# Kernel tuning notes

Measured on AMD Instinct MI355X. Metric: run time of the kernel, lower is better.

The kernel has to match this reference:

```python
import jax, jax.numpy as jnp
import numpy as np

B, N, DM, H = 2, 512, 1024, 16  # batch, seq, d_model, n_heads
DEPTHS = [1, 2, 4, 8]
LAM = 0.1  # lambda_distance


def setup_inputs() -> dict:
    key = jax.random.key(0)
    ks = jax.random.split(key, 2 + 5 * len(DEPTHS))
    inp = {
        "x": jax.random.normal(ks[0], (B, N, DM), jnp.float32),
        "depth_logits": jax.random.normal(ks[1], (len(DEPTHS),), jnp.float32),
    }
    j = 2
    for i, D in enumerate(DEPTHS):
        ds = DM // D
        r = max(1, D // 4)
        inp[f"pe{i}"] = jax.random.normal(ks[j], (N, D, ds), jnp.float32) * 0.02; j += 1
        inp[f"wqkv{i}"] = jax.random.normal(ks[j], (D, ds, 3 * ds), jnp.float32) / np.sqrt(ds); j += 1
        inp[f"wo{i}"] = jax.random.normal(ks[j], (DM, DM), jnp.float32) / np.sqrt(DM); j += 1
        inp[f"fu{i}"] = jax.random.normal(ks[j], (D, r), jnp.float32) / np.sqrt(r); j += 1
        inp[f"fv{i}"] = jax.random.normal(ks[j], (r, D), jnp.float32); j += 1
    return inp


def _ring_bias(n, lam, dtype):
    # toroidal (circular) distance bias on the sequence ring, normalized by N/2
    idx = jnp.arange(n)
    diff = jnp.abs(idx[:, None] - idx[None, :])
    ring = jnp.minimum(diff, n - diff).astype(dtype)
    return -lam * ring * (2.0 / n)  # [N, N]


def _toroidal_branch(x, pe, wqkv, wo, fu, fv):
    # x: [B, N, DM]; pe: [N, D, ds]; wqkv: [D, ds, 3ds]; wo: [DM, DM]; fu@fv: [D, D]
    b, n, dm = x.shape
    d_depth, ds, _ = wqkv.shape
    hd = ds // H
    xs = x.reshape(b, n, d_depth, ds) + pe[None]          # [B, N, D, ds]
    qkv = jnp.einsum('bnds,dse->bnde', xs, wqkv)          # per-depth-slice projection
    q, k, v = jnp.split(qkv, 3, axis=-1)
    q = q.reshape(b, n, d_depth, H, hd)
    k = k.reshape(b, n, d_depth, H, hd)
    v = v.reshape(b, n, d_depth, H, hd)
    bias = _ring_bias(n, LAM, x.dtype)
    scores = jnp.einsum('bndhe,bmdhe->bdhnm', q, k) / jnp.sqrt(jnp.asarray(hd, x.dtype))
    attn = jax.nn.softmax(scores + bias, axis=-1)          # [B, D, H, N, N]
    o = jnp.einsum('bdhnm,bmdhe->bndhe', attn, v).reshape(b, n, d_depth, ds)
    mix = fu @ fv                                          # low-rank depth fusion [D, D]
    fused = jnp.einsum('df,bnfs->bnds', mix, o).reshape(b, n, dm)
    return fused @ wo


def _forward(x, depth_logits, pe0, wqkv0, wo0, fu0, fv0, pe1, wqkv1, wo1, fu1, fv1,
             pe2, wqkv2, wo2, fu2, fv2, pe3, wqkv3, wo3, fu3, fv3):
    # inference-mode depth selection: hard one-hot at argmax (all branches still computed)
    w = jax.nn.one_hot(jnp.argmax(depth_logits), depth_logits.shape[0], dtype=x.dtype)
    params = [(pe0, wqkv0, wo0, fu0, fv0), (pe1, wqkv1, wo1, fu1, fv1),
              (pe2, wqkv2, wo2, fu2, fv2), (pe3, wqkv3, wo3, fu3, fv3)]
    out = jnp.zeros_like(x)
    for i, p in enumerate(params):
        out = out + w[i] * _toroidal_branch(x, *p)
    return out


def reference(x, depth_logits, pe0, wqkv0, wo0, fu0, fv0, pe1, wqkv1, wo1, fu1, fv1,
              pe2, wqkv2, wo2, fu2, fv2, pe3, wqkv3, wo3, fu3, fv3):
    return _forward(x, depth_logits, pe0, wqkv0, wo0, fu0, fv0, pe1, wqkv1, wo1, fu1, fv1,
                    pe2, wqkv2, wo2, fu2, fv2, pe3, wqkv3, wo3, fu3, fv3)
```

## Files before the change

### kernel.cpp

```cpp
#include <hip/hip_runtime.h>

#define B_   2
#define N_   512
#define DM_  1024
#define H_   16
#define LAM_ 0.1f

typedef __attribute__((ext_vector_type(8))) short bf16x8;
typedef __attribute__((ext_vector_type(4))) float f32x4;
typedef unsigned short ush;
struct ush4 { ush x, y, z, w; };
struct uint2s { unsigned x, y; };

__device__ inline ush f2bf(float v) {
    union { float f; unsigned u; } c; c.f = v;
    unsigned r = c.u + 0x7FFF + ((c.u >> 16) & 1);
    return (ush)(r >> 16);
}
__device__ inline float bf2f(ush b) {
    union { float f; unsigned u; } c; c.u = ((unsigned)b) << 16; return c.f;
}
__device__ inline f32x4 mfma16(bf16x8 a, bf16x8 b, f32x4 c) {
    return __builtin_amdgcn_mfma_f32_16x16x32_bf16(a, b, c, 0, 0, 0);
}

template<int HD> struct vpad_t { static constexpr int PT = (HD >= 16) ? HD + 16 : 16; };

__global__ void k_select(const float* __restrict__ logits, int* __restrict__ sel) {
    if (threadIdx.x == 0) {
        float best = logits[0]; int bi = 0;
        for (int i = 1; i < 4; ++i) { float v = logits[i]; if (v > best) { best = v; bi = i; } }
        *sel = bi;
    }
}

template<int D>
__device__ void prep_wt_tile(int bT, int tid, const float* __restrict__ w,
                             ush* __restrict__ wh, ush* __restrict__ wl,
                             float (*lds)[65]) {
    constexpr int ds = DM_ / D;
    constexpr int tpr = 3 * ds / 64;
    constexpr int tpc = ds / 64;
    constexpr int tpd = tpr * tpc;
    if (bT >= D * tpd) return;
    const int d = bT / tpd, rem = bT % tpd;
    const int tr = rem / tpr, tc = rem % tpr;
    const float* src = w + (size_t)d * ds * 3 * ds;
    ush* dsth = wh + (size_t)d * 3 * ds * ds;
    ush* dstl = wl + (size_t)d * 3 * ds * ds;
    const int c = tid & 63, r0 = tid >> 6;
    #pragma unroll
    for (int j = 0; j < 16; ++j) {
        const int r = j * 4 + r0;
        lds[r][c] = src[(size_t)(tr * 64 + r) * (3 * ds) + tc * 64 + c];
    }
    __syncthreads();
    #pragma unroll
    for (int j = 0; j < 16; ++j) {
        const int r = j * 4 + r0;
        const float v = lds[c][r];
        const size_t o = (size_t)(tc * 64 + r) * ds + tr * 64 + c;
        const ush h = f2bf(v);
        dsth[o] = h; dstl[o] = f2bf(v - bf2f(h));
    }
}
template<int D>
__device__ void prep_vpad(int bT, int tid, ush* __restrict__ Vth, ush* __restrict__ Vtl) {
    constexpr int ds = DM_ / D, hd = ds / H_;
    constexpr int PT = vpad_t<hd>::PT;
    constexpr int NH = B_ * D * H_;
    constexpr int PR = PT - hd;
    constexpr int TOT = NH * PR * (N_ / 4);
    const int g = bT * 256 + tid;
    if (g >= TOT) return;
    constexpr int perh = PR * (N_ / 4);
    const int head = g / perh, rem = g % perh;
    const int r = hd + rem / (N_ / 4), n4 = (rem % (N_ / 4)) * 4;
    const size_t o = ((size_t)head * PT + r) * N_ + n4;
    const ush one = (r == hd) ? (ush)0x3F80 : (ush)0;
    ush4 hv; hv.x = one; hv.y = one; hv.z = one; hv.w = one;
    ush4 zv; zv.x = 0; zv.y = 0; zv.z = 0; zv.w = 0;
    *(ush4*)&Vth[o] = hv;
    *(ush4*)&Vtl[o] = zv;
}
__global__ __launch_bounds__(256) void k_prep(
        const int* __restrict__ sel, const float* __restrict__ x,
        const float* __restrict__ pe0, const float* __restrict__ pe1,
        const float* __restrict__ pe2, const float* __restrict__ pe3,
        const float* __restrict__ w0, const float* __restrict__ w1,
        const float* __restrict__ w2, const float* __restrict__ w3,
        const float* __restrict__ wo0, const float* __restrict__ wo1,
        const float* __restrict__ wo2, const float* __restrict__ wo3,
        ush* __restrict__ xh, ush* __restrict__ xl,
        ush* __restrict__ wqh, ush* __restrict__ wql,
        ush* __restrict__ woh, ush* __restrict__ wol,
        ush* __restrict__ Vth, ush* __restrict__ Vtl) {
    __shared__ float lds[64][65];
    const int s = *sel;
    const int bid = blockIdx.x, tid = threadIdx.x;
    if (bid < 1024) {
        const float* pe = (s == 0) ? pe0 : (s == 1) ? pe1 : (s == 2) ? pe2 : pe3;
        const size_t i0 = ((size_t)bid * 256 + tid) * 4;
        const float4 xv = *(const float4*)&x[i0];
        const float4 pv = *(const float4*)&pe[i0 & ((size_t)N_ * DM_ - 1)];
        ush4 h4, l4;
        float v;
        v = xv.x + pv.x; h4.x = f2bf(v); l4.x = f2bf(v - bf2f(h4.x));
        v = xv.y + pv.y; h4.y = f2bf(v); l4.y = f2bf(v - bf2f(h4.y));
        v = xv.z + pv.z; h4.z = f2bf(v); l4.z = f2bf(v - bf2f(h4.z));
        v = xv.w + pv.w; h4.w = f2bf(v); l4.w = f2bf(v - bf2f(h4.w));
        *(ush4*)&xh[i0] = h4;
        *(ush4*)&xl[i0] = l4;
    } else if (bid < 1792) {
        const int bT = bid - 1024;
        switch (s) {
            case 0: prep_wt_tile<1>(bT, tid, w0, wqh, wql, lds); break;
            case 1: prep_wt_tile<2>(bT, tid, w1, wqh, wql, lds); break;
            case 2: prep_wt_tile<4>(bT, tid, w2, wqh, wql, lds); break;
            case 3: prep_wt_tile<8>(bT, tid, w3, wqh, wql, lds); break;
        }
    } else if (bid < 2048) {
        const float* w = (s == 0) ? wo0 : (s == 1) ? wo1 : (s == 2) ? wo2 : wo3;
        const int bT = bid - 1792;
        const int tr = bT >> 4, tc = bT & 15;
        const int c = tid & 63, r0 = tid >> 6;
        #pragma unroll
        for (int j = 0; j < 16; ++j) {
            const int r = j * 4 + r0;
            lds[r][c] = w[(size_t)(tr * 64 + r) * DM_ + tc * 64 + c];
        }
        __syncthreads();
        #pragma unroll
        for (int j = 0; j < 16; ++j) {
            const int r = j * 4 + r0;
            const float v = lds[c][r];
            const size_t o = (size_t)(tc * 64 + r) * DM_ + tr * 64 + c;
            const ush h = f2bf(v);
            woh[o] = h; wol[o] = f2bf(v - bf2f(h));
        }
    } else {
        const int bT = bid - 2048;
        switch (s) {
            case 0: prep_vpad<1>(bT, tid, Vth, Vtl); break;
            case 1: prep_vpad<2>(bT, tid, Vth, Vtl); break;
            case 2: prep_vpad<4>(bT, tid, Vth, Vtl); break;
            case 3: prep_vpad<8>(bT, tid, Vth, Vtl); break;
        }
    }
}

template<int KD>
__device__ void gemm_core(const ush* __restrict__ Ah, const ush* __restrict__ Al, int lda,
                          const ush* __restrict__ Bh, const ush* __restrict__ Bl, int ldb,
                          int row0, int col0, int tid, ush* lds, f32x4 acc[2][2]) {
    ush* lAh = lds; ush* lAl = lds + 2560; ush* lBh = lds + 5120; ush* lBl = lds + 7680;
    const int srow = tid >> 2, scg = tid & 3;
    const int lane = tid & 63, w = tid >> 6;
    const int wm = w >> 1, wn = w & 1;
    const int lr = lane & 15, lb = lane >> 4;

    for (int k0 = 0; k0 < KD; k0 += 32) {
        *(bf16x8*)&lAh[srow * 40 + scg * 8] =
            *(const bf16x8*)&Ah[(size_t)(row0 + srow) * lda + k0 + scg * 8];
        *(bf16x8*)&lAl[srow * 40 + scg * 8] =
            *(const bf16x8*)&Al[(size_t)(row0 + srow) * lda + k0 + scg * 8];
        *(bf16x8*)&lBh[srow * 40 + scg * 8] =
            *(const bf16x8*)&Bh[(size_t)(col0 + srow) * ldb + k0 + scg * 8];
        *(bf16x8*)&lBl[srow * 40 + scg * 8] =
            *(const bf16x8*)&Bl[(size_t)(col0 + srow) * ldb + k0 + scg * 8];
        __syncthreads();
        bf16x8 ah[2], al[2], bh[2], bl[2];
        #pragma unroll
        for (int mg = 0; mg < 2; ++mg) {
            const int r = wm * 32 + mg * 16 + lr;
            ah[mg] = *(const bf16x8*)&lAh[r * 40 + lb * 8];
            al[mg] = *(const bf16x8*)&lAl[r * 40 + lb * 8];
        }
        #pragma unroll
        for (int ng = 0; ng < 2; ++ng) {
            const int r = wn * 32 + ng * 16 + lr;
            bh[ng] = *(const bf16x8*)&lBh[r * 40 + lb * 8];
            bl[ng] = *(const bf16x8*)&lBl[r * 40 + lb * 8];
        }
        #pragma unroll
        for (int mg = 0; mg < 2; ++mg)
            #pragma unroll
            for (int ng = 0; ng < 2; ++ng) {
                acc[mg][ng] = mfma16(ah[mg], bh[ng], acc[mg][ng]);
                acc[mg][ng] = mfma16(al[mg], bh[ng], acc[mg][ng]);
                acc[mg][ng] = mfma16(ah[mg], bl[ng], acc[mg][ng]);
            }
        __syncthreads();
    }
}

template<int D>
__device__ void qkv_body(int bid, int tid,
                         const ush* __restrict__ xh, const ush* __restrict__ xl,
                         const ush* __restrict__ wh, const ush* __restrict__ wl,
                         ush* __restrict__ Qh, ush* __restrict__ Ql,
                         ush* __restrict__ Kh, ush* __restrict__ Kl,
                         ush* __restrict__ Vth, ush* __restrict__ Vtl, ush* lds) {
    constexpr int ds = DM_ / D;
    constexpr int hd = ds / H_;
    constexpr int PT = vpad_t<hd>::PT;
    constexpr int nx = 3 * ds / 64;
    const int bx = bid % nx, by = (bid / nx) & 7, bz = bid / (nx * 8);
    const int b = bz / D, d = bz % D;
    const int row0 = by * 64, col0 = bx * 64;

    f32x4 acc[2][2] = {};
    gemm_core<ds>(xh + (size_t)b * N_ * DM_ + d * ds, xl + (size_t)b * N_ * DM_ + d * ds, DM_,
                  wh + (size_t)d * 3 * ds * ds, wl + (size_t)d * 3 * ds * ds, ds,
                  row0, col0, tid, lds, acc);

    const int lane = tid & 63, w = tid >> 6;
    const int wm = w >> 1, wn = w & 1;
    const int lr = lane & 15, lb = lane >> 4;
    #pragma unroll
    for (int mg = 0; mg < 2; ++mg)
        #pragma unroll
        for (int ng = 0; ng < 2; ++ng) {
            const int n0 = row0 + wm * 32 + mg * 16 + lb * 4;
            const int e  = col0 + wn * 32 + ng * 16 + lr;
            const int part = e / ds, ep = e % ds;
            const int h = ep / hd, t = ep % hd;
            const size_t head = ((size_t)b * D + d) * H_ + h;
            if (part == 2) {
                ush4 h4, l4;
                const float v0 = acc[mg][ng][0], v1 = acc[mg][ng][1];
                const float v2 = acc[mg][ng][2], v3 = acc[mg][ng][3];
                h4.x = f2bf(v0); l4.x = f2bf(v0 - bf2f(h4.x));
                h4.y = f2bf(v1); l4.y = f2bf(v1 - bf2f(h4.y));
                h4.z = f2bf(v2); l4.z = f2bf(v2 - bf2f(h4.z));
                h4.w = f2bf(v3); l4.w = f2bf(v3 - bf2f(h4.w));
                const size_t o = (head * PT + t) * N_ + n0;
                *(ush4*)&Vth[o] = h4;
                *(ush4*)&Vtl[o] = l4;
            } else {
                #pragma unroll
                for (int i = 0; i < 4; ++i) {
                    const size_t o = (head * N_ + n0 + i) * hd + t;
                    const float v = acc[mg][ng][i];
                    const ush hh = f2bf(v), ll = f2bf(v - bf2f(hh));
                    if (part == 0) { Qh[o] = hh; Ql[o] = ll; }
                    else           { Kh[o] = hh; Kl[o] = ll; }
                }
            }
        }
}
__global__ __launch_bounds__(256) void k_qkv(
        const int* __restrict__ sel,
        const ush* __restrict__ xh, const ush* __restrict__ xl,
        const ush* __restrict__ wh, const ush* __restrict__ wl,
        ush* __restrict__ Qh, ush* __restrict__ Ql,
        ush* __restrict__ Kh, ush* __restrict__ Kl,
        ush* __restrict__ Vth, ush* __restrict__ Vtl) {
    __shared__ ush lds[4 * 2560];
    const int bid = blockIdx.x, tid = threadIdx.x;
    switch (*sel) {
        case 0: qkv_body<1>(bid, tid, xh, xl, wh, wl, Qh, Ql, Kh, Kl, Vth, Vtl, lds); break;
        case 1: qkv_body<2>(bid, tid, xh, xl, wh, wl, Qh, Ql, Kh, Kl, Vth, Vtl, lds); break;
        case 2: qkv_body<4>(bid, tid, xh, xl, wh, wl, Qh, Ql, Kh, Kl, Vth, Vtl, lds); break;
        case 3: qkv_body<8>(bid, tid, xh, xl, wh, wl, Qh, Ql, Kh, Kl, Vth, Vtl, lds); break;
    }
}

template<int D>
__device__ void attn_dev(int bid, int tid,
        const ush* __restrict__ Qh, const ush* __restrict__ Ql,
        const ush* __restrict__ Kh, const ush* __restrict__ Kl,
        const ush* __restrict__ Vth, const ush* __restrict__ Vtl,
        float* __restrict__ O, ush* Pall) {
    constexpr int ds = DM_ / D, hd = ds / H_;
    constexpr int CH  = (hd >= 64) ? 2 : 1;
    constexpr int NTP = (hd >= 16) ? hd / 16 + 1 : 1;
    constexpr int PT  = vpad_t<hd>::PT;
    constexpr int TL  = hd / 16;
    constexpr int LRL = hd % 16;
    constexpr int NBLK = B_ * D * H_ * 8;
    if (bid >= NBLK) return;
    const int bidr = (bid & 7) * (NBLK / 8) + (bid >> 3);
    const int w = tid >> 6;
    const int gw = bidr * 4 + w;
    const int head = gw >> 5, qt = gw & 31;
    const int h = head % H_, d = (head / H_) % D, b = head / (H_ * D);
    const int q0 = qt * 16;
    const size_t hbq = (size_t)head * N_ * hd;
    const size_t hbv = (size_t)head * PT * N_;
    const int lane = tid & 63, lr = lane & 15, lb = lane >> 4;
    ush* Pc = Pall + w * 16 * 40;
    const float L2E = 1.44269504f;
    const float SC  = rsqrtf((float)hd) * L2E;
    const float RB2 = LAM_ * (2.0f / N_) * L2E;
    const bf16x8 z8 = {0, 0, 0, 0, 0, 0, 0, 0};

    bf16x8 qah[CH], qal[CH];
    #pragma unroll
    for (int c = 0; c < CH; ++c) {
        const int k0 = c * 32 + lb * 8;
        bf16x8 vh = z8, vl = z8;
        if (k0 < hd) {
            const size_t o = hbq + (size_t)(q0 + lr) * hd + k0;
            vh = *(const bf16x8*)&Qh[o];
            vl = *(const bf16x8*)&Ql[o];
        }
        qah[c] = vh; qal[c] = vl;
    }

    const int q = q0 + lr;
    f32x4 acc2[NTP];
    #pragma unroll
    for (int tt = 0; tt < NTP; ++tt) acc2[tt] = (f32x4){0.f, 0.f, 0.f, 0.f};

    for (int ck = 0; ck < 16; ++ck) {
        const int col0 = ck * 32;

        f32x4 s0 = {0.f, 0.f, 0.f, 0.f}, s1 = {0.f, 0.f, 0.f, 0.f};
        #pragma unroll
        for (int c = 0; c < CH; ++c) {
            const int k0 = c * 32 + lb * 8;
            bf16x8 k0h = z8, k0l = z8, k1h = z8, k1l = z8;
            if (k0 < hd) {
                const size_t o0 = hbq + (size_t)(col0 + lr) * hd + k0;
                const size_t o1 = hbq + (size_t)(col0 + 16 + lr) * hd + k0;
                k0h = *(const bf16x8*)&Kh[o0]; k0l = *(const bf16x8*)&Kl[o0];
                k1h = *(const bf16x8*)&Kh[o1]; k1l = *(const bf16x8*)&Kl[o1];
            }
            s0 = mfma16(k0h, qah[c], s0);
            s0 = mfma16(k0l, qah[c], s0);
            s0 = mfma16(k0h, qal[c], s0);
            s1 = mfma16(k1h, qah[c], s1);
            s1 = mfma16(k1l, qah[c], s1);
            s1 = mfma16(k1h, qal[c], s1);
        }

        #pragma unroll
        for (int t = 0; t < 2; ++t) {
            const f32x4 sv = t ? s1 : s0;
            const int kbase = col0 + t * 16 + lb * 4;
            float p[4];
            #pragma unroll
            for (int i = 0; i < 4; ++i) {
                int dd = q - (kbase + i); dd = dd < 0 ? -dd : dd;
                const int ring = (dd < N_ - dd) ? dd : (N_ - dd);
                p[i] = exp2f(sv[i] * SC - RB2 * (float)ring);
            }
            unsigned pk0, pk1;
            asm("v_cvt_pk_bf16_f32 %0, %1, %2" : "=v"(pk0) : "v"(p[0]), "v"(p[1]));
            asm("v_cvt_pk_bf16_f32 %0, %1, %2" : "=v"(pk1) : "v"(p[2]), "v"(p[3]));
            uint2s pv; pv.x = pk0; pv.y = pk1;
            *(uint2s*)((char*)Pc + lr * 80 + t * 32 + lb * 8) = pv;
        }

        const bf16x8 pa = *(const bf16x8*)((const char*)Pc + lr * 80 + lb * 16);
        #pragma unroll
        for (int tt = 0; tt < NTP; ++tt) {
            const size_t o = hbv + (size_t)(tt * 16 + lr) * N_ + col0 + lb * 8;
            const bf16x8 vh8 = *(const bf16x8*)&Vth[o];
            const bf16x8 vl8 = *(const bf16x8*)&Vtl[o];
            acc2[tt] = mfma16(pa, vh8, acc2[tt]);
            acc2[tt] = mfma16(pa, vl8, acc2[tt]);
        }
    }

    float linv[4];
    #pragma unroll
    for (int i = 0; i < 4; ++i)
        linv[i] = 1.0f / __shfl(acc2[TL][i], (lane & 48) | LRL);

    #pragma unroll
    for (int tt = 0; tt < NTP; ++tt)
        #pragma unroll
        for (int i = 0; i < 4; ++i) {
            const int rn = q0 + lb * 4 + i;
            const int tc = tt * 16 + lr;
            if (tc < hd)
                O[((size_t)b * N_ + rn) * DM_ + d * ds + h * hd + tc] = acc2[tt][i] * linv[i];
        }
}
#define DEF_ATTN(NAME, DD, BR)                                                \
__global__ __launch_bounds__(256) void NAME(                                  \
        const int* __restrict__ sel,                                          \
        const ush* __restrict__ Qh, const ush* __restrict__ Ql,               \
        const ush* __restrict__ Kh, const ush* __restrict__ Kl,               \
        const ush* __restrict__ Vth, const ush* __restrict__ Vtl,             \
        float* __restrict__ O) {                                              \
    __shared__ __align__(16) ush Pc[4 * 16 * 40];                             \
    if (*sel != BR) return;                                                   \
    attn_dev<DD>(blockIdx.x, threadIdx.x, Qh, Ql, Kh, Kl, Vth, Vtl, O, Pc);   \
}
DEF_ATTN(k_attn_1, 1, 0)
DEF_ATTN(k_attn_2, 2, 1)
DEF_ATTN(k_attn_4, 4, 2)
DEF_ATTN(k_attn_8, 8, 3)

template<int D>
__device__ void mix_body(int bid, int tid, const float* __restrict__ fu,
                         const float* __restrict__ fv, const float* __restrict__ O,
                         ush* __restrict__ Fh, ush* __restrict__ Fl, float* mixs) {
    constexpr int ds = DM_ / D;
    constexpr int R = (D / 4 > 0) ? (D / 4) : 1;
    if (tid < D * D) {
        const int d = tid / D, f = tid % D;
        float m = 0.f;
        #pragma unroll
        for (int rr = 0; rr < R; ++rr) m += fu[d * R + rr] * fv[rr * D + f];
        mixs[tid] = m;
    }
    __syncthreads();
    const size_t idx = (size_t)bid * 256 + tid;
    const int dm = (int)(idx % DM_);
    const size_t bn = idx / DM_;
    const int d = dm / ds, s0 = dm % ds;
    const float* Ob = O + bn * DM_ + s0;
    float acc = 0.f;
    #pragma unroll
    for (int f = 0; f < D; ++f) acc += mixs[d * D + f] * Ob[(size_t)f * ds];
    const ush hh = f2bf(acc);
    Fh[idx] = hh; Fl[idx] = f2bf(acc - bf2f(hh));
}
__global__ __launch_bounds__(256) void k_mix(
        const int* __restrict__ sel,
        const float* __restrict__ fu0, const float* __restrict__ fv0,
        const float* __restrict__ fu1, const float* __restrict__ fv1,
        const float* __restrict__ fu2, const float* __restrict__ fv2,
        const float* __restrict__ fu3, const float* __restrict__ fv3,
        const float* __restrict__ O, ush* __restrict__ Fh, ush* __restrict__ Fl) {
    __shared__ float mixs[64];
    const int bid = blockIdx.x, tid = threadIdx.x;
    switch (*sel) {
        case 0: mix_body<1>(bid, tid, fu0, fv0, O, Fh, Fl, mixs); break;
        case 1: mix_body<2>(bid, tid, fu1, fv1, O, Fh, Fl, mixs); break;
        case 2: mix_body<4>(bid, tid, fu2, fv2, O, Fh, Fl, mixs); break;
        case 3: mix_body<8>(bid, tid, fu3, fv3, O, Fh, Fl, mixs); break;
    }
}

__global__ __launch_bounds__(256) void k_wo(
        const ush* __restrict__ Fh, const ush* __restrict__ Fl,
        const ush* __restrict__ wh, const ush* __restrict__ wl,
        float* __restrict__ out) {
    __shared__ ush lA[2][32 * 40];
    __shared__ ush lB[2][64 * 40];
    const int tid = threadIdx.x;
    const int bx = blockIdx.x & 15, by = blockIdx.x >> 4;
    const int row0 = by * 32, col0 = bx * 64;
    const int lane = tid & 63, w = tid >> 6;
    const int wq = w >> 1, wn = w & 1;
    const int lr = lane & 15, lb = lane >> 4;
    f32x4 acc[2] = {};

    for (int k0 = 0; k0 < DM_; k0 += 32) {
        {
            const int half = tid >> 7, t2 = tid & 127;
            const int srow = t2 >> 2, scg = t2 & 3;
            const ush* src = half ? Fl : Fh;
            *(bf16x8*)&lA[half][srow * 40 + scg * 8] =
                *(const bf16x8*)&src[(size_t)(row0 + srow) * DM_ + k0 + scg * 8];
        }
        {
            const int srow = tid >> 2, scg = tid & 3;
            *(bf16x8*)&lB[0][srow * 40 + scg * 8] =
                *(const bf16x8*)&wh[(size_t)(col0 + srow) * DM_ + k0 + scg * 8];
            *(bf16x8*)&lB[1][srow * 40 + scg * 8] =
                *(const bf16x8*)&wl[(size_t)(col0 + srow) * DM_ + k0 + scg * 8];
        }
        __syncthreads();
        const int ar = wq * 16 + lr;
        const bf16x8 ah = *(const bf16x8*)&lA[0][ar * 40 + lb * 8];
        const bf16x8 al = *(const bf16x8*)&lA[1][ar * 40 + lb * 8];
        #pragma unroll
        for (int ng = 0; ng < 2; ++ng) {
            const int br = wn * 32 + ng * 16 + lr;
            const bf16x8 bh = *(const bf16x8*)&lB[0][br * 40 + lb * 8];
            const bf16x8 bl = *(const bf16x8*)&lB[1][br * 40 + lb * 8];
            acc[ng] = mfma16(ah, bh, acc[ng]);
            acc[ng] = mfma16(al, bh, acc[ng]);
            acc[ng] = mfma16(ah, bl, acc[ng]);
        }
        __syncthreads();
    }
    #pragma unroll
    for (int ng = 0; ng < 2; ++ng)
        #pragma unroll
        for (int i = 0; i < 4; ++i) {
            const int r = row0 + wq * 16 + lb * 4 + i;
            const int c = col0 + wn * 32 + ng * 16 + lr;
            out[(size_t)r * DM_ + c] = acc[ng][i];
        }
}

extern "C" void kernel_launch(void* const* d_in, const int* in_sizes, int n_in,
                              void* d_out, int out_size, void* d_ws, size_t ws_size,
                              hipStream_t stream) {
    const float* x      = (const float*)d_in[0];
    const float* logits = (const float*)d_in[1];
    float* out = (float*)d_out;

    char* p = (char*)d_ws;
    int* sel = (int*)p; p += 256;
    const size_t MB = 1024 * 1024;
    ush* Qh = (ush*)p; p += 2 * MB;
    ush* Ql = (ush*)p; p += 2 * MB;
    ush* Kh = (ush*)p; p += 2 * MB;
    ush* Kl = (ush*)p; p += 2 * MB;
    ush* Vth = (ush*)p; p += 4 * MB;
    ush* Vtl = (ush*)p; p += 4 * MB;
    float* O = (float*)p; p += 4 * MB;
    ush* xh = (ush*)p; p += 2 * MB;
    ush* xl = (ush*)p; p += 2 * MB;
    ush* wqh = (ush*)p; p += 6 * MB;
    ush* wql = (ush*)p; p += 6 * MB;
    ush* woh = (ush*)p; p += 2 * MB;
    ush* wol = (ush*)p; p += 2 * MB;
    ush* Fh = xh, *Fl = xl;

    k_select<<<1, 64, 0, stream>>>(logits, sel);
    k_prep<<<dim3(3072), dim3(256), 0, stream>>>(
        sel, x,
        (const float*)d_in[2], (const float*)d_in[7],
        (const float*)d_in[12], (const float*)d_in[17],
        (const float*)d_in[3], (const float*)d_in[8],
        (const float*)d_in[13], (const float*)d_in[18],
        (const float*)d_in[4], (const float*)d_in[9],
        (const float*)d_in[14], (const float*)d_in[19],
        xh, xl, wqh, wql, woh, wol, Vth, Vtl);
    k_qkv<<<dim3(768), dim3(256), 0, stream>>>(sel, xh, xl, wqh, wql,
                                               Qh, Ql, Kh, Kl, Vth, Vtl);
    k_attn_1<<<dim3(256),  dim3(256), 0, stream>>>(sel, Qh, Ql, Kh, Kl, Vth, Vtl, O);
    k_attn_2<<<dim3(512),  dim3(256), 0, stream>>>(sel, Qh, Ql, Kh, Kl, Vth, Vtl, O);
    k_attn_4<<<dim3(1024), dim3(256), 0, stream>>>(sel, Qh, Ql, Kh, Kl, Vth, Vtl, O);
    k_attn_8<<<dim3(2048), dim3(256), 0, stream>>>(sel, Qh, Ql, Kh, Kl, Vth, Vtl, O);
    k_mix<<<dim3(B_ * N_ * DM_ / 256), dim3(256), 0, stream>>>(
        sel,
        (const float*)d_in[5],  (const float*)d_in[6],
        (const float*)d_in[10], (const float*)d_in[11],
        (const float*)d_in[15], (const float*)d_in[16],
        (const float*)d_in[20], (const float*)d_in[21],
        O, Fh, Fl);
    k_wo<<<dim3(512), dim3(256), 0, stream>>>(Fh, Fl, woh, wol, out);
}
```

Before: 98.13 us.

## Split attention key range across wave pairs, precompute ring bias table, fold Q scale

Each 16-row query tile is now handled by two waves, each covering half of the keys. Their partial P·V sums are combined through shared memory before normalisation, which doubles the block count and the parallelism. The ring-distance bias becomes a per-block shared exp2 table multiplied into exp2(score), and the softmax scale times log2(e) is folded into Q during the QKV projection. The separate argmax kernel is removed and every kernel recomputes the selection from the logits. The costs are an extra block barrier, additional shared memory, and a reliance on unnormalised exp without max subtraction, as before.

```diff
diff --git a/kernel.cpp b/kernel.cpp
--- a/kernel.cpp
+++ b/kernel.cpp
@@ -23,16 +23,15 @@
 __device__ inline f32x4 mfma16(bf16x8 a, bf16x8 b, f32x4 c) {
     return __builtin_amdgcn_mfma_f32_16x16x32_bf16(a, b, c, 0, 0, 0);
 }
+__device__ inline int sel_of(const float* __restrict__ lg) {
+    float b = lg[0]; int s = 0;
+    if (lg[1] > b) { b = lg[1]; s = 1; }
+    if (lg[2] > b) { b = lg[2]; s = 2; }
+    if (lg[3] > b) { b = lg[3]; s = 3; }
+    return s;
+}
 
 template<int HD> struct vpad_t { static constexpr int PT = (HD >= 16) ? HD + 16 : 16; };
-
-__global__ void k_select(const float* __restrict__ logits, int* __restrict__ sel) {
-    if (threadIdx.x == 0) {
-        float best = logits[0]; int bi = 0;
-        for (int i = 1; i < 4; ++i) { float v = logits[i]; if (v > best) { best = v; bi = i; } }
-        *sel = bi;
-    }
-}
 
 template<int D>
 __device__ void prep_wt_tile(int bT, int tid, const float* __restrict__ w,
@@ -84,7 +83,7 @@
     *(ush4*)&Vtl[o] = zv;
 }
 __global__ __launch_bounds__(256) void k_prep(
-        const int* __restrict__ sel, const float* __restrict__ x,
+        const float* __restrict__ logits, const float* __restrict__ x,
         const float* __restrict__ pe0, const float* __restrict__ pe1,
         const float* __restrict__ pe2, const float* __restrict__ pe3,
         const float* __restrict__ w0, const float* __restrict__ w1,
@@ -96,7 +95,7 @@
         ush* __restrict__ woh, ush* __restrict__ wol,
         ush* __restrict__ Vth, ush* __restrict__ Vtl) {
     __shared__ float lds[64][65];
-    const int s = *sel;
+    const int s = sel_of(logits);
     const int bid = blockIdx.x, tid = threadIdx.x;
     if (bid < 1024) {
         const float* pe = (s == 0) ? pe0 : (s == 1) ? pe1 : (s == 2) ? pe2 : pe3;
@@ -208,6 +207,7 @@
     const int bx = bid % nx, by = (bid / nx) & 7, bz = bid / (nx * 8);
     const int b = bz / D, d = bz % D;
     const int row0 = by * 64, col0 = bx * 64;
+    const float SCQ = 1.44269504f * rsqrtf((float)hd);
 
     f32x4 acc[2][2] = {};
     gemm_core<ds>(xh + (size_t)b * N_ * DM_ + d * ds, xl + (size_t)b * N_ * DM_ + d * ds, DM_,
@@ -241,7 +241,8 @@
                 #pragma unroll
                 for (int i = 0; i < 4; ++i) {
                     const size_t o = (head * N_ + n0 + i) * hd + t;
-                    const float v = acc[mg][ng][i];
+                    float v = acc[mg][ng][i];
+                    if (part == 0) v *= SCQ;
                     const ush hh = f2bf(v), ll = f2bf(v - bf2f(hh));
                     if (part == 0) { Qh[o] = hh; Ql[o] = ll; }
                     else           { Kh[o] = hh; Kl[o] = ll; }
@@ -250,7 +251,7 @@
         }
 }
 __global__ __launch_bounds__(256) void k_qkv(
-        const int* __restrict__ sel,
+        const float* __restrict__ logits,
         const ush* __restrict__ xh, const ush* __restrict__ xl,
         const ush* __restrict__ wh, const ush* __restrict__ wl,
         ush* __restrict__ Qh, ush* __restrict__ Ql,
@@ -258,7 +259,7 @@
         ush* __restrict__ Vth, ush* __restrict__ Vtl) {
     __shared__ ush lds[4 * 2560];
     const int bid = blockIdx.x, tid = threadIdx.x;
-    switch (*sel) {
+    switch (sel_of(logits)) {
         case 0: qkv_body<1>(bid, tid, xh, xl, wh, wl, Qh, Ql, Kh, Kl, Vth, Vtl, lds); break;
         case 1: qkv_body<2>(bid, tid, xh, xl, wh, wl, Qh, Ql, Kh, Kl, Vth, Vtl, lds); break;
         case 2: qkv_body<4>(bid, tid, xh, xl, wh, wl, Qh, Ql, Kh, Kl, Vth, Vtl, lds); break;
@@ -271,28 +272,34 @@
         const ush* __restrict__ Qh, const ush* __restrict__ Ql,
         const ush* __restrict__ Kh, const ush* __restrict__ Kl,
         const ush* __restrict__ Vth, const ush* __restrict__ Vtl,
-        float* __restrict__ O, ush* Pall) {
+        float* __restrict__ O, ush* Pall, float* wtab, float* comb) {
     constexpr int ds = DM_ / D, hd = ds / H_;
     constexpr int CH  = (hd >= 64) ? 2 : 1;
     constexpr int NTP = (hd >= 16) ? hd / 16 + 1 : 1;
     constexpr int PT  = vpad_t<hd>::PT;
     constexpr int TL  = hd / 16;
     constexpr int LRL = hd % 16;
-    constexpr int NBLK = B_ * D * H_ * 8;
-    if (bid >= NBLK) return;
+    constexpr int NBLK = B_ * D * H_ * 16;
+    const float RB2 = LAM_ * (2.0f / N_) * 1.44269504f;
+
+    for (int j = tid; j < 516; j += 256) {
+        const int jj = j & 511;
+        const int ring = (jj < 512 - jj) ? jj : 512 - jj;
+        wtab[j] = exp2f(-RB2 * (float)ring);
+    }
+    __syncthreads();
+
     const int bidr = (bid & 7) * (NBLK / 8) + (bid >> 3);
-    const int w = tid >> 6;
-    const int gw = bidr * 4 + w;
-    const int head = gw >> 5, qt = gw & 31;
+    const int w = tid >> 6, lane = tid & 63;
+    const int pair = w >> 1, half = w & 1;
+    const int gt = bidr * 2 + pair;
+    const int head = gt >> 5, qt = gt & 31;
     const int h = head % H_, d = (head / H_) % D, b = head / (H_ * D);
     const int q0 = qt * 16;
     const size_t hbq = (size_t)head * N_ * hd;
     const size_t hbv = (size_t)head * PT * N_;
-    const int lane = tid & 63, lr = lane & 15, lb = lane >> 4;
+    const int lr = lane & 15, lb = lane >> 4;
     ush* Pc = Pall + w * 16 * 40;
-    const float L2E = 1.44269504f;
-    const float SC  = rsqrtf((float)hd) * L2E;
-    const float RB2 = LAM_ * (2.0f / N_) * L2E;
     const bf16x8 z8 = {0, 0, 0, 0, 0, 0, 0, 0};
 
     bf16x8 qah[CH], qal[CH];
@@ -313,7 +320,7 @@
     #pragma unroll
     for (int tt = 0; tt < NTP; ++tt) acc2[tt] = (f32x4){0.f, 0.f, 0.f, 0.f};
 
-    for (int ck = 0; ck < 16; ++ck) {
+    for (int ck = half * 8; ck < half * 8 + 8; ++ck) {
         const int col0 = ck * 32;
 
         f32x4 s0 = {0.f, 0.f, 0.f, 0.f}, s1 = {0.f, 0.f, 0.f, 0.f};
@@ -339,13 +346,11 @@
         for (int t = 0; t < 2; ++t) {
             const f32x4 sv = t ? s1 : s0;
             const int kbase = col0 + t * 16 + lb * 4;
+            const int j0 = (kbase - q) & 511;
             float p[4];
             #pragma unroll
-            for (int i = 0; i < 4; ++i) {
-                int dd = q - (kbase + i); dd = dd < 0 ? -dd : dd;
-                const int ring = (dd < N_ - dd) ? dd : (N_ - dd);
-                p[i] = exp2f(sv[i] * SC - RB2 * (float)ring);
-            }
+            for (int i = 0; i < 4; ++i)
+                p[i] = exp2f(sv[i]) * wtab[j0 + i];
             unsigned pk0, pk1;
             asm("v_cvt_pk_bf16_f32 %0, %1, %2" : "=v"(pk0) : "v"(p[0]), "v"(p[1]));
             asm("v_cvt_pk_bf16_f32 %0, %1, %2" : "=v"(pk1) : "v"(p[2]), "v"(p[3]));
@@ -364,31 +369,48 @@
         }
     }
 
-    float linv[4];
-    #pragma unroll
-    for (int i = 0; i < 4; ++i)
-        linv[i] = 1.0f / __shfl(acc2[TL][i], (lane & 48) | LRL);
-
-    #pragma unroll
-    for (int tt = 0; tt < NTP; ++tt)
-        #pragma unroll
-        for (int i = 0; i < 4; ++i) {
-            const int rn = q0 + lb * 4 + i;
-            const int tc = tt * 16 + lr;
-            if (tc < hd)
-                O[((size_t)b * N_ + rn) * DM_ + d * ds + h * hd + tc] = acc2[tt][i] * linv[i];
-        }
+    if (half) {
+        #pragma unroll
+        for (int tt = 0; tt < NTP; ++tt)
+            #pragma unroll
+            for (int i = 0; i < 4; ++i)
+                comb[((pair * NTP + tt) * 4 + i) * 64 + lane] = acc2[tt][i];
+    }
+    __syncthreads();
+    if (!half) {
+        #pragma unroll
+        for (int tt = 0; tt < NTP; ++tt)
+            #pragma unroll
+            for (int i = 0; i < 4; ++i)
+                acc2[tt][i] += comb[((pair * NTP + tt) * 4 + i) * 64 + lane];
+        float linv[4];
+        #pragma unroll
+        for (int i = 0; i < 4; ++i)
+            linv[i] = 1.0f / __shfl(acc2[TL][i], (lane & 48) | LRL);
+        #pragma unroll
+        for (int tt = 0; tt < NTP; ++tt)
+            #pragma unroll
+            for (int i = 0; i < 4; ++i) {
+                const int rn = q0 + lb * 4 + i;
+                const int tc = tt * 16 + lr;
+                if (tc < hd)
+                    O[((size_t)b * N_ + rn) * DM_ + d * ds + h * hd + tc] = acc2[tt][i] * linv[i];
+            }
+    }
 }
 #define DEF_ATTN(NAME, DD, BR)                                                \
 __global__ __launch_bounds__(256) void NAME(                                  \
-        const int* __restrict__ sel,                                          \
+        const float* __restrict__ logits,                                     \
         const ush* __restrict__ Qh, const ush* __restrict__ Ql,               \
         const ush* __restrict__ Kh, const ush* __restrict__ Kl,               \
         const ush* __restrict__ Vth, const ush* __restrict__ Vtl,             \
         float* __restrict__ O) {                                              \
     __shared__ __align__(16) ush Pc[4 * 16 * 40];                             \
-    if (*sel != BR) return;                                                   \
-    attn_dev<DD>(blockIdx.x, threadIdx.x, Qh, Ql, Kh, Kl, Vth, Vtl, O, Pc);   \
+    __shared__ float wtab[516];                                               \
+    __shared__ float comb[2560];                                              \
+    if (sel_of(logits) != BR) return;                                         \
+    attn_dev<DD>(blockIdx.x, threadIdx.x, Qh, Ql, Kh, Kl, Vth, Vtl, O,        \
+                 Pc, wtab, comb);                                             \
 }
 DEF_ATTN(k_attn_1, 1, 0)
 DEF_ATTN(k_attn_2, 2, 1)
@@ -421,7 +443,7 @@
     Fh[idx] = hh; Fl[idx] = f2bf(acc - bf2f(hh));
 }
 __global__ __launch_bounds__(256) void k_mix(
-        const int* __restrict__ sel,
+        const float* __restrict__ logits,
         const float* __restrict__ fu0, const float* __restrict__ fv0,
         const float* __restrict__ fu1, const float* __restrict__ fv1,
         const float* __restrict__ fu2, const float* __restrict__ fv2,
@@ -429,7 +451,7 @@
         const float* __restrict__ O, ush* __restrict__ Fh, ush* __restrict__ Fl) {
     __shared__ float mixs[64];
     const int bid = blockIdx.x, tid = threadIdx.x;
-    switch (*sel) {
+    switch (sel_of(logits)) {
         case 0: mix_body<1>(bid, tid, fu0, fv0, O, Fh, Fl, mixs); break;
         case 1: mix_body<2>(bid, tid, fu1, fv1, O, Fh, Fl, mixs); break;
         case 2: mix_body<4>(bid, tid, fu2, fv2, O, Fh, Fl, mixs); break;
@@ -499,7 +521,7 @@
     float* out = (float*)d_out;
 
     char* p = (char*)d_ws;
-    int* sel = (int*)p; p += 256;
+    p += 256;
     const size_t MB = 1024 * 1024;
     ush* Qh = (ush*)p; p += 2 * MB;
     ush* Ql = (ush*)p; p += 2 * MB;
@@ -516,9 +538,8 @@
     ush* wol = (ush*)p; p += 2 * MB;
     ush* Fh = xh, *Fl = xl;
 
-    k_select<<<1, 64, 0, stream>>>(logits, sel);
     k_prep<<<dim3(3072), dim3(256), 0, stream>>>(
-        sel, x,
+        logits, x,
         (const float*)d_in[2], (const float*)d_in[7],
         (const float*)d_in[12], (const float*)d_in[17],
         (const float*)d_in[3], (const float*)d_in[8],
@@ -526,14 +547,14 @@
         (const float*)d_in[4], (const float*)d_in[9],
         (const float*)d_in[14], (const float*)d_in[19],
         xh, xl, wqh, wql, woh, wol, Vth, Vtl);
-    k_qkv<<<dim3(768), dim3(256), 0, stream>>>(sel, xh, xl, wqh, wql,
+    k_qkv<<<dim3(768), dim3(256), 0, stream>>>(logits, xh, xl, wqh, wql,
                                                Qh, Ql, Kh, Kl, Vth, Vtl);
-    k_attn_1<<<dim3(256),  dim3(256), 0, stream>>>(sel, Qh, Ql, Kh, Kl, Vth, Vtl, O);
-    k_attn_2<<<dim3(512),  dim3(256), 0, stream>>>(sel, Qh, Ql, Kh, Kl, Vth, Vtl, O);
-    k_attn_4<<<dim3(1024), dim3(256), 0, stream>>>(sel, Qh, Ql, Kh, Kl, Vth, Vtl, O);
-    k_attn_8<<<dim3(2048), dim3(256), 0, stream>>>(sel, Qh, Ql, Kh, Kl, Vth, Vtl, O);
+    k_attn_1<<<dim3(512),  dim3(256), 0, stream>>>(logits, Qh, Ql, Kh, Kl, Vth, Vtl, O);
+    k_attn_2<<<dim3(1024), dim3(256), 0, stream>>>(logits, Qh, Ql, Kh, Kl, Vth, Vtl, O);
+    k_attn_4<<<dim3(2048), dim3(256), 0, stream>>>(logits, Qh, Ql, Kh, Kl, Vth, Vtl, O);
+    k_attn_8<<<dim3(4096), dim3(256), 0, stream>>>(logits, Qh, Ql, Kh, Kl, Vth, Vtl, O);
     k_mix<<<dim3(B_ * N_ * DM_ / 256), dim3(256), 0, stream>>>(
-        sel,
+        logits,
         (const float*)d_in[5],  (const float*)d_in[6],
         (const float*)d_in[10], (const float*)d_in[11],
         (const float*)d_in[15], (const float*)d_in[16],
```

Measured after the change: 99.31 us. Within noise of the previous version (+1.2%).

## Fuse depth mix into Wo GEMM, inline argmax, prescale Q

Applied to the files above, without the earlier changes.

Removes the k_select kernel by computing the argmax of the depth logits inline in every kernel. Drops the standalone k_mix kernel and instead computes the low-rank depth mix on the fly while loading the A tile of the Wo GEMM, splitting it into bf16 hi/lo there. This saves two launches and the F round-trip through memory. It also folds the softmax scale and log2e into Q at QKV write time. The cost is that each Wo block recomputes the mix for its A tile, with a runtime loop over Dv and gathered fp32 reads of O, and only half the threads do that staging work.

```diff
diff --git a/kernel.cpp b/kernel.cpp
--- a/kernel.cpp
+++ b/kernel.cpp
@@ -23,16 +23,15 @@
 __device__ inline f32x4 mfma16(bf16x8 a, bf16x8 b, f32x4 c) {
     return __builtin_amdgcn_mfma_f32_16x16x32_bf16(a, b, c, 0, 0, 0);
 }
+__device__ inline int sel_of(const float* __restrict__ lg) {
+    float b = lg[0]; int s = 0;
+    if (lg[1] > b) { b = lg[1]; s = 1; }
+    if (lg[2] > b) { b = lg[2]; s = 2; }
+    if (lg[3] > b) { b = lg[3]; s = 3; }
+    return s;
+}
 
 template<int HD> struct vpad_t { static constexpr int PT = (HD >= 16) ? HD + 16 : 16; };
-
-__global__ void k_select(const float* __restrict__ logits, int* __restrict__ sel) {
-    if (threadIdx.x == 0) {
-        float best = logits[0]; int bi = 0;
-        for (int i = 1; i < 4; ++i) { float v = logits[i]; if (v > best) { best = v; bi = i; } }
-        *sel = bi;
-    }
-}
 
 template<int D>
 __device__ void prep_wt_tile(int bT, int tid, const float* __restrict__ w,
@@ -84,7 +83,7 @@
     *(ush4*)&Vtl[o] = zv;
 }
 __global__ __launch_bounds__(256) void k_prep(
-        const int* __restrict__ sel, const float* __restrict__ x,
+        const float* __restrict__ logits, const float* __restrict__ x,
         const float* __restrict__ pe0, const float* __restrict__ pe1,
         const float* __restrict__ pe2, const float* __restrict__ pe3,
         const float* __restrict__ w0, const float* __restrict__ w1,
@@ -96,7 +95,7 @@
         ush* __restrict__ woh, ush* __restrict__ wol,
         ush* __restrict__ Vth, ush* __restrict__ Vtl) {
     __shared__ float lds[64][65];
-    const int s = *sel;
+    const int s = sel_of(logits);
     const int bid = blockIdx.x, tid = threadIdx.x;
     if (bid < 1024) {
         const float* pe = (s == 0) ? pe0 : (s == 1) ? pe1 : (s == 2) ? pe2 : pe3;
@@ -208,6 +207,7 @@
     const int bx = bid % nx, by = (bid / nx) & 7, bz = bid / (nx * 8);
     const int b = bz / D, d = bz % D;
     const int row0 = by * 64, col0 = bx * 64;
+    const float SCQ = 1.44269504f * rsqrtf((float)hd);
 
     f32x4 acc[2][2] = {};
     gemm_core<ds>(xh + (size_t)b * N_ * DM_ + d * ds, xl + (size_t)b * N_ * DM_ + d * ds, DM_,
@@ -241,7 +241,8 @@
                 #pragma unroll
                 for (int i = 0; i < 4; ++i) {
                     const size_t o = (head * N_ + n0 + i) * hd + t;
-                    const float v = acc[mg][ng][i];
+                    float v = acc[mg][ng][i];
+                    if (part == 0) v *= SCQ;
                     const ush hh = f2bf(v), ll = f2bf(v - bf2f(hh));
                     if (part == 0) { Qh[o] = hh; Ql[o] = ll; }
                     else           { Kh[o] = hh; Kl[o] = ll; }
@@ -250,7 +251,7 @@
         }
 }
 __global__ __launch_bounds__(256) void k_qkv(
-        const int* __restrict__ sel,
+        const float* __restrict__ logits,
         const ush* __restrict__ xh, const ush* __restrict__ xl,
         const ush* __restrict__ wh, const ush* __restrict__ wl,
         ush* __restrict__ Qh, ush* __restrict__ Ql,
@@ -258,7 +259,7 @@
         ush* __restrict__ Vth, ush* __restrict__ Vtl) {
     __shared__ ush lds[4 * 2560];
     const int bid = blockIdx.x, tid = threadIdx.x;
-    switch (*sel) {
+    switch (sel_of(logits)) {
         case 0: qkv_body<1>(bid, tid, xh, xl, wh, wl, Qh, Ql, Kh, Kl, Vth, Vtl, lds); break;
         case 1: qkv_body<2>(bid, tid, xh, xl, wh, wl, Qh, Ql, Kh, Kl, Vth, Vtl, lds); break;
         case 2: qkv_body<4>(bid, tid, xh, xl, wh, wl, Qh, Ql, Kh, Kl, Vth, Vtl, lds); break;
@@ -290,9 +291,7 @@
     const size_t hbv = (size_t)head * PT * N_;
     const int lane = tid & 63, lr = lane & 15, lb = lane >> 4;
     ush* Pc = Pall + w * 16 * 40;
-    const float L2E = 1.44269504f;
-    const float SC  = rsqrtf((float)hd) * L2E;
-    const float RB2 = LAM_ * (2.0f / N_) * L2E;
+    const float RB2 = LAM_ * (2.0f / N_) * 1.44269504f;
     const bf16x8 z8 = {0, 0, 0, 0, 0, 0, 0, 0};
 
     bf16x8 qah[CH], qal[CH];
@@ -344,7 +343,7 @@
             for (int i = 0; i < 4; ++i) {
                 int dd = q - (kbase + i); dd = dd < 0 ? -dd : dd;
                 const int ring = (dd < N_ - dd) ? dd : (N_ - dd);
-                p[i] = exp2f(sv[i] * SC - RB2 * (float)ring);
+                p[i] = exp2f(sv[i] - RB2 * (float)ring);
             }
             unsigned pk0, pk1;
             asm("v_cvt_pk_bf16_f32 %0, %1, %2" : "=v"(pk0) : "v"(p[0]), "v"(p[1]));
@@ -381,13 +380,13 @@
 }
 #define DEF_ATTN(NAME, DD, BR)                                                \
 __global__ __launch_bounds__(256) void NAME(                                  \
-        const int* __restrict__ sel,                                          \
+        const float* __restrict__ logits,                                     \
         const ush* __restrict__ Qh, const ush* __restrict__ Ql,               \
         const ush* __restrict__ Kh, const ush* __restrict__ Kl,               \
         const ush* __restrict__ Vth, const ush* __restrict__ Vtl,             \
         float* __restrict__ O) {                                              \
     __shared__ __align__(16) ush Pc[4 * 16 * 40];                             \
-    if (*sel != BR) return;                                                   \
+    if (sel_of(logits) != BR) return;                                         \
     attn_dev<DD>(blockIdx.x, threadIdx.x, Qh, Ql, Kh, Kl, Vth, Vtl, O, Pc);   \
 }
 DEF_ATTN(k_attn_1, 1, 0)
@@ -395,55 +394,38 @@
 DEF_ATTN(k_attn_4, 4, 2)
 DEF_ATTN(k_attn_8, 8, 3)
 
-template<int D>
-__device__ void mix_body(int bid, int tid, const float* __restrict__ fu,
-                         const float* __restrict__ fv, const float* __restrict__ O,
-                         ush* __restrict__ Fh, ush* __restrict__ Fl, float* mixs) {
-    constexpr int ds = DM_ / D;
-    constexpr int R = (D / 4 > 0) ? (D / 4) : 1;
-    if (tid < D * D) {
-        const int d = tid / D, f = tid % D;
-        float m = 0.f;
-        #pragma unroll
-        for (int rr = 0; rr < R; ++rr) m += fu[d * R + rr] * fv[rr * D + f];
-        mixs[tid] = m;
-    }
-    __syncthreads();
-    const size_t idx = (size_t)bid * 256 + tid;
-    const int dm = (int)(idx % DM_);
-    const size_t bn = idx / DM_;
-    const int d = dm / ds, s0 = dm % ds;
-    const float* Ob = O + bn * DM_ + s0;
-    float acc = 0.f;
-    #pragma unroll
-    for (int f = 0; f < D; ++f) acc += mixs[d * D + f] * Ob[(size_t)f * ds];
-    const ush hh = f2bf(acc);
-    Fh[idx] = hh; Fl[idx] = f2bf(acc - bf2f(hh));
-}
-__global__ __launch_bounds__(256) void k_mix(
-        const int* __restrict__ sel,
+__global__ __launch_bounds__(256) void k_wo(
+        const float* __restrict__ logits,
         const float* __restrict__ fu0, const float* __restrict__ fv0,
         const float* __restrict__ fu1, const float* __restrict__ fv1,
         const float* __restrict__ fu2, const float* __restrict__ fv2,
         const float* __restrict__ fu3, const float* __restrict__ fv3,
-        const float* __restrict__ O, ush* __restrict__ Fh, ush* __restrict__ Fl) {
-    __shared__ float mixs[64];
-    const int bid = blockIdx.x, tid = threadIdx.x;
-    switch (*sel) {
-        case 0: mix_body<1>(bid, tid, fu0, fv0, O, Fh, Fl, mixs); break;
-        case 1: mix_body<2>(bid, tid, fu1, fv1, O, Fh, Fl, mixs); break;
-        case 2: mix_body<4>(bid, tid, fu2, fv2, O, Fh, Fl, mixs); break;
-        case 3: mix_body<8>(bid, tid, fu3, fv3, O, Fh, Fl, mixs); break;
-    }
-}
-
-__global__ __launch_bounds__(256) void k_wo(
-        const ush* __restrict__ Fh, const ush* __restrict__ Fl,
+        const float* __restrict__ O,
         const ush* __restrict__ wh, const ush* __restrict__ wl,
         float* __restrict__ out) {
     __shared__ ush lA[2][32 * 40];
     __shared__ ush lB[2][64 * 40];
+    __shared__ float mixs[64];
     const int tid = threadIdx.x;
+    const int s = sel_of(logits);
+    int Dv, dsh;
+    const float *fu, *fv;
+    switch (s) {
+        case 0:  Dv = 1; dsh = 10; fu = fu0; fv = fv0; break;
+        case 1:  Dv = 2; dsh = 9;  fu = fu1; fv = fv1; break;
+        case 2:  Dv = 4; dsh = 8;  fu = fu2; fv = fv2; break;
+        default: Dv = 8; dsh = 7;  fu = fu3; fv = fv3; break;
+    }
+    const int Rv = (Dv / 4 > 0) ? (Dv / 4) : 1;
+    const int dmask = (1 << dsh) - 1;
+    if (tid < Dv * Dv) {
+        const int d = tid / Dv, f = tid % Dv;
+        float m = 0.f;
+        for (int rr = 0; rr < Rv; ++rr) m += fu[d * Rv + rr] * fv[rr * Dv + f];
+        mixs[tid] = m;
+    }
+    __syncthreads();
+
     const int bx = blockIdx.x & 15, by = blockIdx.x >> 4;
     const int row0 = by * 32, col0 = bx * 64;
     const int lane = tid & 63, w = tid >> 6;
@@ -452,12 +434,23 @@
     f32x4 acc[2] = {};
 
     for (int k0 = 0; k0 < DM_; k0 += 32) {
-        {
-            const int half = tid >> 7, t2 = tid & 127;
-            const int srow = t2 >> 2, scg = t2 & 3;
-            const ush* src = half ? Fl : Fh;
-            *(bf16x8*)&lA[half][srow * 40 + scg * 8] =
-                *(const bf16x8*)&src[(size_t)(row0 + srow) * DM_ + k0 + scg * 8];
+        if (tid < 128) {
+            const int srow = tid >> 2, scg = tid & 3;
+            const float* Orow = O + (size_t)(row0 + srow) * DM_;
+            bf16x8 hv, lv;
+            #pragma unroll
+            for (int j = 0; j < 8; ++j) {
+                const int kk = k0 + scg * 8 + j;
+                const int dd = kk >> dsh, ss = kk & dmask;
+                float a = 0.f;
+                for (int f = 0; f < Dv; ++f)
+                    a += mixs[dd * Dv + f] * Orow[(f << dsh) + ss];
+                const ush hh = f2bf(a);
+                hv[j] = (short)hh;
+                lv[j] = (short)f2bf(a - bf2f(hh));
+            }
+            *(bf16x8*)&lA[0][srow * 40 + scg * 8] = hv;
+            *(bf16x8*)&lA[1][srow * 40 + scg * 8] = lv;
         }
         {
             const int srow = tid >> 2, scg = tid & 3;
@@ -499,7 +492,7 @@
     float* out = (float*)d_out;
 
     char* p = (char*)d_ws;
-    int* sel = (int*)p; p += 256;
+    p += 256;
     const size_t MB = 1024 * 1024;
     ush* Qh = (ush*)p; p += 2 * MB;
     ush* Ql = (ush*)p; p += 2 * MB;
@@ -514,11 +507,9 @@
     ush* wql = (ush*)p; p += 6 * MB;
     ush* woh = (ush*)p; p += 2 * MB;
     ush* wol = (ush*)p; p += 2 * MB;
-    ush* Fh = xh, *Fl = xl;
-
-    k_select<<<1, 64, 0, stream>>>(logits, sel);
+
     k_prep<<<dim3(3072), dim3(256), 0, stream>>>(
-        sel, x,
+        logits, x,
         (const float*)d_in[2], (const float*)d_in[7],
         (const float*)d_in[12], (const float*)d_in[17],
         (const float*)d_in[3], (const float*)d_in[8],
@@ -526,18 +517,17 @@
         (const float*)d_in[4], (const float*)d_in[9],
         (const float*)d_in[14], (const float*)d_in[19],
         xh, xl, wqh, wql, woh, wol, Vth, Vtl);
-    k_qkv<<<dim3(768), dim3(256), 0, stream>>>(sel, xh, xl, wqh, wql,
+    k_qkv<<<dim3(768), dim3(256), 0, stream>>>(logits, xh, xl, wqh, wql,
                                                Qh, Ql, Kh, Kl, Vth, Vtl);
-    k_attn_1<<<dim3(256),  dim3(256), 0, stream>>>(sel, Qh, Ql, Kh, Kl, Vth, Vtl, O);
-    k_attn_2<<<dim3(512),  dim3(256), 0, stream>>>(sel, Qh, Ql, Kh, Kl, Vth, Vtl, O);
-    k_attn_4<<<dim3(1024), dim3(256), 0, stream>>>(sel, Qh, Ql, Kh, Kl, Vth, Vtl, O);
-    k_attn_8<<<dim3(2048), dim3(256), 0, stream>>>(sel, Qh, Ql, Kh, Kl, Vth, Vtl, O);
-    k_mix<<<dim3(B_ * N_ * DM_ / 256), dim3(256), 0, stream>>>(
-        sel,
+    k_attn_1<<<dim3(256),  dim3(256), 0, stream>>>(logits, Qh, Ql, Kh, Kl, Vth, Vtl, O);
+    k_attn_2<<<dim3(512),  dim3(256), 0, stream>>>(logits, Qh, Ql, Kh, Kl, Vth, Vtl, O);
+    k_attn_4<<<dim3(1024), dim3(256), 0, stream>>>(logits, Qh, Ql, Kh, Kl, Vth, Vtl, O);
+    k_attn_8<<<dim3(2048), dim3(256), 0, stream>>>(logits, Qh, Ql, Kh, Kl, Vth, Vtl, O);
+    k_wo<<<dim3(512), dim3(256), 0, stream>>>(
+        logits,
         (const float*)d_in[5],  (const float*)d_in[6],
         (const float*)d_in[10], (const float*)d_in[11],
         (const float*)d_in[15], (const float*)d_in[16],
         (const float*)d_in[20], (const float*)d_in[21],
-        O, Fh, Fl);
-    k_wo<<<dim3(512), dim3(256), 0, stream>>>(Fh, Fl, woh, wol, out);
-}
+        O, woh, wol, out);
+}
```

New measurement: 215.8 us. 120% more time.
